# Optimization experiments

Hardware: AMD Instinct MI355X
Metric: run time of the kernel (lower is better)

Reference implementation:

```python
import jax, jax.numpy as jnp
import numpy as np
from jax import lax

B, C_IN, N, K = 4, 128, 4096, 16
C_OUT = 256
EPS = 1e-5


def setup_inputs() -> dict:
    key = jax.random.key(0)
    k1, k2, k3, k4, k5 = jax.random.split(key, 5)
    x = jax.random.normal(k1, (B, C_IN, N, 1), dtype=jnp.float32)
    y = jax.random.normal(k2, (B, C_IN, N, 1), dtype=jnp.float32)
    edge_index = jax.random.randint(k3, (2, B, N, K), 0, N)
    # Conv2d(in=2*C_IN, out=C_OUT, kernel 3x3), kaiming-ish scale
    fan_in = 2 * C_IN * 9
    conv_w = jax.random.normal(k4, (C_OUT, 2 * C_IN, 3, 3), dtype=jnp.float32) * (2.0 / fan_in) ** 0.5
    conv_b = jnp.zeros((C_OUT,), dtype=jnp.float32)
    gamma = jnp.ones((C_OUT,), dtype=jnp.float32)
    beta = jnp.zeros((C_OUT,), dtype=jnp.float32)
    _ = k5
    return {"x": x, "y": y, "edge_index": edge_index,
            "conv_w": conv_w, "conv_b": conv_b, "gamma": gamma, "beta": beta}


def _batched_index_select(feat, idx):
    # feat: [B, C, N, 1], idx: [B, N, K] -> [B, C, N, K]
    fs = feat[..., 0]  # [B, C, N]
    return jax.vmap(lambda fb, ib: fb[:, ib])(fs, idx)


def reference(x, y, edge_index, conv_w, conv_b, gamma, beta):
    x_i = _batched_index_select(x, edge_index[1])        # [B, C, N, K]
    x_j = _batched_index_select(y, edge_index[0])        # [B, C, N, K]
    h = jnp.concatenate([x_i, x_j - x_i], axis=1)        # [B, 2C, N, K]
    out = lax.conv_general_dilated(
        h, conv_w, window_strides=(1, 1), padding=((1, 1), (1, 1)),
        dimension_numbers=("NCHW", "OIHW", "NCHW"))
    out = out + conv_b[None, :, None, None]
    # BatchNorm2d in training mode: biased batch statistics per channel
    mean = jnp.mean(out, axis=(0, 2, 3), keepdims=True)
    var = jnp.mean((out - mean) ** 2, axis=(0, 2, 3), keepdims=True)
    out = gamma[None, :, None, None] * (out - mean) * lax.rsqrt(var + EPS) + beta[None, :, None, None]
    out = jax.nn.relu(out)
    return jnp.max(out, axis=-1, keepdims=True)          # [B, C_OUT, N, 1]
```

## Files before the change

kernel.cpp:

```cpp
#include <hip/hip_runtime.h>

typedef unsigned short u16;
typedef unsigned int u32;
typedef __attribute__((ext_vector_type(8))) u16 u16x8;
typedef __attribute__((ext_vector_type(8))) __bf16 bf16x8;
typedef __attribute__((ext_vector_type(4))) float f32x4;

#define CIN 128
#define NB 4
#define NN 4096
#define KPTS 16
#define COUT 256
#define POSB 65536
#define TOTPOS 262144
#define CK 2304

__device__ __forceinline__ float bf2f(u16 u){ return __uint_as_float(((u32)u)<<16); }
__device__ __forceinline__ u16 f2bf(float f){
  u32 u = __float_as_uint(f);
  u32 r = (u + 0x7fffu + ((u>>16)&1u)) >> 16;
  return (u16)r;
}

__global__ void pack_w_kernel(const float* __restrict__ w, u16* __restrict__ wp){
  int t = blockIdx.x*256 + threadIdx.x;
  if (t >= COUT*CK) return;
  int co = t / CK; int r = t - co*CK; int tap = r >> 8; int c = r & 255;
  float v;
  if (c < 128)
    v = w[(co*256 + c)*9 + tap] - w[(co*256 + 128 + c)*9 + tap];
  else
    v = w[(co*256 + c)*9 + tap];
  wp[t] = f2bf(v);
}

__global__ void transpose_cast_kernel(const float* __restrict__ x, const float* __restrict__ y,
                                      u16* __restrict__ xt, u16* __restrict__ yt){
  __shared__ u16 tile[2][32][65];
  int n0 = blockIdx.x*64, c0 = blockIdx.y*32, b = blockIdx.z;
  int t = threadIdx.x;
  int tn = t & 63, tc = t >> 6;
  #pragma unroll
  for (int i=0;i<8;++i){
    int c = tc*8 + i;
    size_t src = ((size_t)(b*CIN + c0 + c))*NN + n0 + tn;
    tile[0][c][tn] = f2bf(x[src]);
    tile[1][c][tn] = f2bf(y[src]);
  }
  __syncthreads();
  int tcc = t & 31, tnn = t >> 5;
  #pragma unroll
  for (int i=0;i<8;++i){
    int n = tnn*8 + i;
    size_t dst = ((size_t)(b*NN + n0 + n))*CIN + c0 + tcc;
    xt[dst] = tile[0][tcc][n];
    yt[dst] = tile[1][tcc][n];
  }
}

#define SWZ(row, chunk) (((row)*32) + ((((chunk) ^ (((row)>>1)&3))) << 3))

__global__ __launch_bounds__(256, 2) void conv_gemm_kernel(const u16* __restrict__ wp,
    const int* __restrict__ e, const u16* __restrict__ xt, const u16* __restrict__ yt,
    const u16* __restrict__ zrow, const float* __restrict__ bias,
    float* __restrict__ ssum, float* __restrict__ ssq, float* __restrict__ maxout){
  __shared__ u16 als[3*8192];
  __shared__ u16 pnl[2*6144];

  int ptile = blockIdx.x;
  int p0 = ptile * 128;
  int b = p0 >> 16;
  int pib0 = p0 & (POSB-1);
  int nb0 = pib0 >> 4;

  int t = threadIdx.x;
  int lane = t & 63, wave = t >> 6;
  int wr = wave >> 1, wc = wave & 1;
  int l15 = lane & 15, l4 = lane >> 4;

  const u16* xb = xt + ((size_t)b)*NN*CIN;
  const u16* yb = yt + ((size_t)b)*NN*CIN;

  int rr = wave*64 + (lane>>2);
  int r0 = rr, r1 = rr+16, r2 = rr+32, r3 = rr+48;
  int ch0 = (lane&3) ^ ((r0>>1)&3);
  int ch1 = (lane&3) ^ ((r1>>1)&3);
  int ch2 = (lane&3) ^ ((r2>>1)&3);
  int ch3 = (lane&3) ^ ((r3>>1)&3);
  int wuni = __builtin_amdgcn_readfirstlane(wave);
  int wu  = wuni*2048;
  int wu2 = wuni*512;
  const u16* pA0 = wp + (size_t)r0*CK + ch0*8;
  const u16* pA1 = wp + (size_t)r1*CK + ch1*8;
  const u16* pA2 = wp + (size_t)r2*CK + ch2*8;
  const u16* pA3 = wp + (size_t)r3*CK + ch3*8;

  const u16 *xp[3], *yp[3];
  { int tq4 = t >> 2;
    #pragma unroll
    for (int i=0;i<3;++i){
      int row = i*64 + tq4;
      int lc = (t&3) ^ ((row>>1)&3);
      int q = (row*57) >> 10;
      int kk = row - q*18 - 1;
      int n2 = nb0 - 1 + q;
      bool valid = (row < 180) && ((unsigned)n2 < (unsigned)NN) && ((unsigned)kk < (unsigned)KPTS);
      int j0 = 0, j1 = 0;
      if (valid){ int eo = b*POSB + n2*16 + kk; j0 = e[eo]; j1 = e[TOTPOS + eo]; }
      xp[i] = (valid ? xb + (size_t)j1*CIN : zrow) + lc*8;
      yp[i] = (valid ? yb + (size_t)j0*CIN : zrow) + lc*8;
    }
  }

  auto G16 = [&](const u16* g, const u16* l){
    __builtin_amdgcn_global_load_lds((const __attribute__((address_space(1))) u32*)g,
                                     (__attribute__((address_space(3))) u32*)l, 16, 0, 0);
  };

  f32x4 acc[8][4];
  #pragma unroll
  for (int i=0;i<8;++i)
    #pragma unroll
    for (int j=0;j<4;++j) acc[i][j] = (f32x4){0.f,0.f,0.f,0.f};

  G16(xp[0],    &pnl[wu2]);
  G16(xp[1],    &pnl[2048+wu2]);
  G16(xp[2],    &pnl[4096+wu2]);
  G16(xp[0]+32, &pnl[6144+wu2]);
  G16(xp[1]+32, &pnl[6144+2048+wu2]);
  G16(xp[2]+32, &pnl[6144+4096+wu2]);
  #pragma unroll
  for (int s=0; s<2; ++s){
    G16(pA0+s*256, &als[s*8192+wu]);
    G16(pA1+s*256, &als[s*8192+wu+512]);
    G16(pA2+s*256, &als[s*8192+wu+1024]);
    G16(pA3+s*256, &als[s*8192+wu+1536]);
  }

  int aoff[8];
  #pragma unroll
  for (int f=0; f<8; ++f) aoff[f] = SWZ(wr*128 + f*16 + l15, l4);
  int wc72l15 = wc*72 + l15;

  #define STEP(TAU) { \
    if ((TAU)==1) asm volatile("s_waitcnt vmcnt(7)\n\ts_barrier" ::: "memory"); \
    else          asm volatile("s_waitcnt vmcnt(4)\n\ts_barrier" ::: "memory"); \
    bf16x8 af[8], bv[4]; \
    { const int abase = ((TAU)%3)*8192; \
      _Pragma("unroll") \
      for (int f=0; f<8; ++f) af[f] = *(bf16x8*)&als[abase + aoff[f]]; } \
    { const u16* pb = pnl + (c&1)*6144; \
      const int kbc = ((TAU)/3)*18 + ((TAU)%3); \
      _Pragma("unroll") \
      for (int f=0; f<4; ++f){ int r = wc72l15 + kbc + f*18; \
        bv[f] = *(bf16x8*)&pb[r*32 + ((l4 ^ ((r>>1)&3))<<3)]; } } \
    if ((TAU)==0){ int cc=(c+1)&7; int co32=(cc&3)*32; \
      const u16* s0=(cc<4?xp[0]:yp[0])+co32; \
      const u16* s1=(cc<4?xp[1]:yp[1])+co32; \
      const u16* s2=(cc<4?xp[2]:yp[2])+co32; \
      int pd=((c+1)&1)*6144; \
      G16(s0,&pnl[pd+wu2]); G16(s1,&pnl[pd+2048+wu2]); G16(s2,&pnl[pd+4096+wu2]); } \
    { const int chs = (c + (((TAU)>=7)?1:0)) & 7; \
      const int koff = ((((TAU)+2)%9)*256) + (chs<<5); \
      const int sbase = (((TAU)+2)%3)*8192; \
      G16(pA0 + koff, &als[sbase + wu]); \
      G16(pA1 + koff, &als[sbase + wu + 512]); \
      G16(pA2 + koff, &als[sbase + wu + 1024]); \
      G16(pA3 + koff, &als[sbase + wu + 1536]); } \
    __builtin_amdgcn_s_setprio(1); \
    _Pragma("unroll") \
    for (int fm=0; fm<8; ++fm) \
      _Pragma("unroll") \
      for (int fn=0; fn<4; ++fn) \
        acc[fm][fn] = __builtin_amdgcn_mfma_f32_16x16x32_bf16(af[fm], bv[fn], acc[fm][fn], 0, 0, 0); \
    __builtin_amdgcn_s_setprio(0); \
  }

  for (int c = 0; c < 8; ++c){
    STEP(0) STEP(1) STEP(2) STEP(3) STEP(4) STEP(5) STEP(6) STEP(7) STEP(8)
  }
  #undef STEP

  asm volatile("s_waitcnt vmcnt(0)\n\ts_barrier" ::: "memory");

  float* fs = (float*)&als[0];
  fs[t] = 0.f; fs[256 + t] = 0.f;
  __syncthreads();

  #pragma unroll
  for (int fm=0; fm<8; ++fm){
    #pragma unroll
    for (int j=0; j<4; ++j){
      int ch = wr*128 + fm*16 + l4*4 + j;
      float bv2 = bias[ch];
      float s = 0.f, q = 0.f;
      float mv[4];
      #pragma unroll
      for (int fn=0; fn<4; ++fn){
        float v = acc[fm][fn][j] + bv2;
        s += v; q += v*v; mv[fn] = v;
      }
      #pragma unroll
      for (int o=1; o<16; o<<=1){
        s += __shfl_xor(s, o, 64);
        q += __shfl_xor(q, o, 64);
        #pragma unroll
        for (int fn=0; fn<4; ++fn) mv[fn] = fmaxf(mv[fn], __shfl_xor(mv[fn], o, 64));
      }
      if (l15 == 0){
        atomicAdd(&fs[ch], s);
        atomicAdd(&fs[256 + ch], q);
        size_t rowb = ((size_t)(b*COUT + ch)) << 12;
        #pragma unroll
        for (int fn=0; fn<4; ++fn)
          maxout[rowb + nb0 + wc*4 + fn] = mv[fn];
      }
    }
  }
  __syncthreads();
  atomicAdd(&ssum[t], fs[t]);
  atomicAdd(&ssq[t],  fs[256 + t]);
}

__global__ void finalize_stats_kernel(const float* __restrict__ ssum, const float* __restrict__ ssq,
                                      const float* __restrict__ gamma, const float* __restrict__ beta,
                                      float* __restrict__ scale, float* __restrict__ shift){
  int co = threadIdx.x;
  float inv = 1.0f / (float)TOTPOS;
  float mean = ssum[co]*inv;
  float var = ssq[co]*inv - mean*mean;
  float sc = gamma[co] * rsqrtf(var + 1e-5f);
  scale[co] = sc;
  shift[co] = beta[co] - mean*sc;
}

__global__ void bn_finish_kernel(float* __restrict__ out, const float* __restrict__ scale,
                                 const float* __restrict__ shift){
  int t = blockIdx.x*256 + threadIdx.x;
  int co = (t >> 12) & 255;
  float v = out[t];
  out[t] = fmaxf(fmaf(scale[co], v, shift[co]), 0.f);
}

extern "C" void kernel_launch(void* const* d_in, const int* in_sizes, int n_in,
                              void* d_out, int out_size, void* d_ws, size_t ws_size,
                              hipStream_t stream){
  const float* x = (const float*)d_in[0];
  const float* y = (const float*)d_in[1];
  const int*   e = (const int*)d_in[2];
  const float* w = (const float*)d_in[3];
  const float* bias = (const float*)d_in[4];
  const float* gamma = (const float*)d_in[5];
  const float* beta  = (const float*)d_in[6];
  float* out = (float*)d_out;

  char* ws = (char*)d_ws;
  u16*   wp    = (u16*)(ws);
  float* ssum  = (float*)(ws + 1179648);
  float* ssq   = (float*)(ws + 1180672);
  u16*   zrow  = (u16*)(ws + 1181696);
  float* scale = (float*)(ws + 1182720);
  float* shift = (float*)(ws + 1183744);
  u16*   xt    = (u16*)(ws + 1184768);
  u16*   yt    = (u16*)(ws + 5379072);

  hipMemsetAsync(ssum, 0, 3072, stream);

  pack_w_kernel<<<2304, 256, 0, stream>>>(w, wp);
  dim3 tg(NN/64, CIN/32, NB);
  transpose_cast_kernel<<<tg, 256, 0, stream>>>(x, y, xt, yt);
  conv_gemm_kernel<<<2048, 256, 0, stream>>>(wp, e, xt, yt, zrow, bias, ssum, ssq, out);
  finalize_stats_kernel<<<1, COUT, 0, stream>>>(ssum, ssq, gamma, beta, scale, shift);
  bn_finish_kernel<<<out_size/256, 256, 0, stream>>>(out, scale, shift);
}
```

Baseline: 324.0 us.

## Double-buffer MFMA fragments in registers and deepen LDS prefetch to three stages

The conv GEMM main loop now reads the next step's A and B fragments from LDS into a second register set while the current step's MFMAs run, ping-ponging between two fragment buffers. The global-to-LDS prefetch distance grows from two to three stages, so all three A slots are preloaded and the slot/offset arithmetic shifts accordingly. The loop over channel chunks is unrolled by two so the panel buffer pointers become compile-time selections. This aims to hide LDS read latency behind the matrix math, at the cost of more fragment registers and extra lgkmcnt waits at each barrier.

```diff
diff --git a/kernel.cpp b/kernel.cpp
--- a/kernel.cpp
+++ b/kernel.cpp
@@ -130,7 +130,7 @@
   G16(xp[1]+32, &pnl[6144+2048+wu2]);
   G16(xp[2]+32, &pnl[6144+4096+wu2]);
   #pragma unroll
-  for (int s=0; s<2; ++s){
+  for (int s=0; s<3; ++s){
     G16(pA0+s*256, &als[s*8192+wu]);
     G16(pA1+s*256, &als[s*8192+wu+512]);
     G16(pA2+s*256, &als[s*8192+wu+1024]);
@@ -142,27 +142,29 @@
   for (int f=0; f<8; ++f) aoff[f] = SWZ(wr*128 + f*16 + l15, l4);
   int wc72l15 = wc*72 + l15;
 
-  #define STEP(TAU) { \
-    if ((TAU)==1) asm volatile("s_waitcnt vmcnt(7)\n\ts_barrier" ::: "memory"); \
-    else          asm volatile("s_waitcnt vmcnt(4)\n\ts_barrier" ::: "memory"); \
-    bf16x8 af[8], bv[4]; \
-    { const int abase = ((TAU)%3)*8192; \
-      _Pragma("unroll") \
-      for (int f=0; f<8; ++f) af[f] = *(bf16x8*)&als[abase + aoff[f]]; } \
-    { const u16* pb = pnl + (c&1)*6144; \
-      const int kbc = ((TAU)/3)*18 + ((TAU)%3); \
-      _Pragma("unroll") \
-      for (int f=0; f<4; ++f){ int r = wc72l15 + kbc + f*18; \
-        bv[f] = *(bf16x8*)&pb[r*32 + ((l4 ^ ((r>>1)&3))<<3)]; } } \
+  bf16x8 f0_a[8], f0_b[4], f1_a[8], f1_b[4];
+
+  asm volatile("s_waitcnt vmcnt(8)\n\ts_barrier" ::: "memory");
+  #pragma unroll
+  for (int f=0; f<8; ++f) f0_a[f] = *(bf16x8*)&als[aoff[f]];
+  #pragma unroll
+  for (int f=0; f<4; ++f){
+    int r = wc72l15 + f*18;
+    f0_b[f] = *(bf16x8*)&pnl[r*32 + ((l4 ^ ((r>>1)&3))<<3)];
+  }
+
+  #define STEP(TAU, CUR, NXT) { \
+    if ((TAU)==1) asm volatile("s_waitcnt vmcnt(7)\n\ts_waitcnt lgkmcnt(0)\n\ts_barrier" ::: "memory"); \
+    else          asm volatile("s_waitcnt vmcnt(4)\n\ts_waitcnt lgkmcnt(0)\n\ts_barrier" ::: "memory"); \
     if ((TAU)==0){ int cc=(c+1)&7; int co32=(cc&3)*32; \
       const u16* s0=(cc<4?xp[0]:yp[0])+co32; \
       const u16* s1=(cc<4?xp[1]:yp[1])+co32; \
       const u16* s2=(cc<4?xp[2]:yp[2])+co32; \
       int pd=((c+1)&1)*6144; \
       G16(s0,&pnl[pd+wu2]); G16(s1,&pnl[pd+2048+wu2]); G16(s2,&pnl[pd+4096+wu2]); } \
-    { const int chs = (c + (((TAU)>=7)?1:0)) & 7; \
-      const int koff = ((((TAU)+2)%9)*256) + (chs<<5); \
-      const int sbase = (((TAU)+2)%3)*8192; \
+    { const int chs = (c + (((TAU)>=6)?1:0)) & 7; \
+      const int koff = ((((TAU)+3)%9)*256) + (chs<<5); \
+      const int sbase = ((TAU)%3)*8192; \
       G16(pA0 + koff, &als[sbase + wu]); \
       G16(pA1 + koff, &als[sbase + wu + 512]); \
       G16(pA2 + koff, &als[sbase + wu + 1024]); \
@@ -172,16 +174,40 @@
     for (int fm=0; fm<8; ++fm) \
       _Pragma("unroll") \
       for (int fn=0; fn<4; ++fn) \
-        acc[fm][fn] = __builtin_amdgcn_mfma_f32_16x16x32_bf16(af[fm], bv[fn], acc[fm][fn], 0, 0, 0); \
+        acc[fm][fn] = __builtin_amdgcn_mfma_f32_16x16x32_bf16(CUR##_a[fm], CUR##_b[fn], acc[fm][fn], 0, 0, 0); \
     __builtin_amdgcn_s_setprio(0); \
-  }
-
-  for (int c = 0; c < 8; ++c){
-    STEP(0) STEP(1) STEP(2) STEP(3) STEP(4) STEP(5) STEP(6) STEP(7) STEP(8)
+    { const int abase = (((TAU)+1)%3)*8192; \
+      _Pragma("unroll") \
+      for (int f=0; f<8; ++f) NXT##_a[f] = *(bf16x8*)&als[abase + aoff[f]]; } \
+    { const u16* pb = ((TAU)==8) ? pbN : pbC; \
+      const int tn = ((TAU)+1)%9; \
+      const int kbc = (tn/3)*18 + (tn%3); \
+      _Pragma("unroll") \
+      for (int f=0; f<4; ++f){ int r = wc72l15 + kbc + f*18; \
+        NXT##_b[f] = *(bf16x8*)&pb[r*32 + ((l4 ^ ((r>>1)&3))<<3)]; } } \
+  }
+
+  for (int cp = 0; cp < 8; cp += 2){
+    {
+      int c = cp;
+      const u16* pbC = pnl;
+      const u16* pbN = pnl + 6144;
+      STEP(0, f0, f1)  STEP(1, f1, f0)  STEP(2, f0, f1)
+      STEP(3, f1, f0)  STEP(4, f0, f1)  STEP(5, f1, f0)
+      STEP(6, f0, f1)  STEP(7, f1, f0)  STEP(8, f0, f1)
+    }
+    {
+      int c = cp + 1;
+      const u16* pbC = pnl + 6144;
+      const u16* pbN = pnl;
+      STEP(0, f1, f0)  STEP(1, f0, f1)  STEP(2, f1, f0)
+      STEP(3, f0, f1)  STEP(4, f1, f0)  STEP(5, f0, f1)
+      STEP(6, f1, f0)  STEP(7, f0, f1)  STEP(8, f1, f0)
+    }
   }
   #undef STEP
 
-  asm volatile("s_waitcnt vmcnt(0)\n\ts_barrier" ::: "memory");
+  asm volatile("s_waitcnt vmcnt(0)\n\ts_waitcnt lgkmcnt(0)\n\ts_barrier" ::: "memory");
 
   float* fs = (float*)&als[0];
   fs[t] = 0.f; fs[256 + t] = 0.f;
```

After: 336.0 us. 3.7% more time.

## Split MFMA step into halves and prefetch next step's LDS fragments

Applied to the files above, without the earlier changes.

Restructures the GEMM main-loop step into two half-phases. Each phase issues 16 MFMAs while LDS reads for the other half of the A fragments, and for the next step's A and B fragments, are in flight. The B fragments and first A half are preloaded before the loop. The aim is to hide LDS read latency behind matrix-core work, a ping-pong style schedule. In exchange each step now has four barriers instead of one and the vmcnt/buffer-index bookkeeping is more complex, which adds sync overhead and correctness risk around the stage-buffer reuse.

```diff
diff --git a/kernel.cpp b/kernel.cpp
--- a/kernel.cpp
+++ b/kernel.cpp
@@ -142,18 +142,19 @@
   for (int f=0; f<8; ++f) aoff[f] = SWZ(wr*128 + f*16 + l15, l4);
   int wc72l15 = wc*72 + l15;
 
+  bf16x8 af[8], bv[4];
+
+  asm volatile("s_waitcnt vmcnt(4)" ::: "memory");
+  asm volatile("s_barrier" ::: "memory");
+  #pragma unroll
+  for (int f=0; f<4; ++f) af[f] = *(bf16x8*)&als[aoff[f]];
+  #pragma unroll
+  for (int f=0; f<4; ++f){
+    int r = wc72l15 + f*18;
+    bv[f] = *(bf16x8*)&pnl[r*32 + ((l4 ^ ((r>>1)&3))<<3)];
+  }
+
   #define STEP(TAU) { \
-    if ((TAU)==1) asm volatile("s_waitcnt vmcnt(7)\n\ts_barrier" ::: "memory"); \
-    else          asm volatile("s_waitcnt vmcnt(4)\n\ts_barrier" ::: "memory"); \
-    bf16x8 af[8], bv[4]; \
-    { const int abase = ((TAU)%3)*8192; \
-      _Pragma("unroll") \
-      for (int f=0; f<8; ++f) af[f] = *(bf16x8*)&als[abase + aoff[f]]; } \
-    { const u16* pb = pnl + (c&1)*6144; \
-      const int kbc = ((TAU)/3)*18 + ((TAU)%3); \
-      _Pragma("unroll") \
-      for (int f=0; f<4; ++f){ int r = wc72l15 + kbc + f*18; \
-        bv[f] = *(bf16x8*)&pb[r*32 + ((l4 ^ ((r>>1)&3))<<3)]; } } \
     if ((TAU)==0){ int cc=(c+1)&7; int co32=(cc&3)*32; \
       const u16* s0=(cc<4?xp[0]:yp[0])+co32; \
       const u16* s1=(cc<4?xp[1]:yp[1])+co32; \
@@ -167,13 +168,40 @@
       G16(pA1 + koff, &als[sbase + wu + 512]); \
       G16(pA2 + koff, &als[sbase + wu + 1024]); \
       G16(pA3 + koff, &als[sbase + wu + 1536]); } \
+    asm volatile("s_barrier" ::: "memory"); \
+    asm volatile("s_waitcnt lgkmcnt(0)" ::: "memory"); \
     __builtin_amdgcn_s_setprio(1); \
     _Pragma("unroll") \
-    for (int fm=0; fm<8; ++fm) \
+    for (int fm=0; fm<4; ++fm) \
       _Pragma("unroll") \
       for (int fn=0; fn<4; ++fn) \
         acc[fm][fn] = __builtin_amdgcn_mfma_f32_16x16x32_bf16(af[fm], bv[fn], acc[fm][fn], 0, 0, 0); \
     __builtin_amdgcn_s_setprio(0); \
+    asm volatile("s_barrier" ::: "memory"); \
+    { const int abase = ((TAU)%3)*8192; \
+      _Pragma("unroll") \
+      for (int f=4; f<8; ++f) af[f] = *(bf16x8*)&als[abase + aoff[f]]; } \
+    if ((TAU)==0) asm volatile("s_waitcnt vmcnt(7)" ::: "memory"); \
+    else          asm volatile("s_waitcnt vmcnt(4)" ::: "memory"); \
+    asm volatile("s_barrier" ::: "memory"); \
+    asm volatile("s_waitcnt lgkmcnt(0)" ::: "memory"); \
+    __builtin_amdgcn_s_setprio(1); \
+    _Pragma("unroll") \
+    for (int fm=4; fm<8; ++fm) \
+      _Pragma("unroll") \
+      for (int fn=0; fn<4; ++fn) \
+        acc[fm][fn] = __builtin_amdgcn_mfma_f32_16x16x32_bf16(af[fm], bv[fn], acc[fm][fn], 0, 0, 0); \
+    __builtin_amdgcn_s_setprio(0); \
+    asm volatile("s_barrier" ::: "memory"); \
+    { const int abase = (((TAU)+1)%3)*8192; \
+      _Pragma("unroll") \
+      for (int f=0; f<4; ++f) af[f] = *(bf16x8*)&als[abase + aoff[f]]; \
+      const u16* pb = pnl + (((((TAU)==8) ? (c+1) : c)) & 1)*6144; \
+      const int tn = ((TAU)+1)%9; \
+      const int kbc = (tn/3)*18 + (tn%3); \
+      _Pragma("unroll") \
+      for (int f=0; f<4; ++f){ int r = wc72l15 + kbc + f*18; \
+        bv[f] = *(bf16x8*)&pb[r*32 + ((l4 ^ ((r>>1)&3))<<3)]; } } \
   }
 
   for (int c = 0; c < 8; ++c){
@@ -181,7 +209,9 @@
   }
   #undef STEP
 
-  asm volatile("s_waitcnt vmcnt(0)\n\ts_barrier" ::: "memory");
+  asm volatile("s_waitcnt vmcnt(0)" ::: "memory");
+  asm volatile("s_waitcnt lgkmcnt(0)" ::: "memory");
+  asm volatile("s_barrier" ::: "memory");
 
   float* fs = (float*)&als[0];
   fs[t] = 0.f; fs[256 + t] = 0.f;
```

After: 341.9 us. 1.06x slower.

## Split conv GEMM tile across eight waves with halved per-wave accumulators

Applied to the files above, without the earlier changes.

Doubles the GEMM block to 512 threads, so each wave computes a 64x64 output sub-tile instead of 128x64, cutting accumulators per thread from 128 to 64 floats. A-tile and gather-panel loads are redistributed to two 16-byte loads per thread. The activation panel buffers grow to 256 rows, and the wait counts are adjusted to match. Launch bounds now request 4 blocks per CU, which caps registers tightly and risks spills. The larger LDS footprint may also prevent that occupancy from being reached.

```diff
diff --git a/kernel.cpp b/kernel.cpp
--- a/kernel.cpp
+++ b/kernel.cpp
@@ -60,12 +60,12 @@
 
 #define SWZ(row, chunk) (((row)*32) + ((((chunk) ^ (((row)>>1)&3))) << 3))
 
-__global__ __launch_bounds__(256, 2) void conv_gemm_kernel(const u16* __restrict__ wp,
+__global__ __launch_bounds__(512, 4) void conv_gemm_kernel(const u16* __restrict__ wp,
     const int* __restrict__ e, const u16* __restrict__ xt, const u16* __restrict__ yt,
     const u16* __restrict__ zrow, const float* __restrict__ bias,
     float* __restrict__ ssum, float* __restrict__ ssq, float* __restrict__ maxout){
   __shared__ u16 als[3*8192];
-  __shared__ u16 pnl[2*6144];
+  __shared__ u16 pnl[2*8192];
 
   int ptile = blockIdx.x;
   int p0 = ptile * 128;
@@ -81,25 +81,19 @@
   const u16* xb = xt + ((size_t)b)*NN*CIN;
   const u16* yb = yt + ((size_t)b)*NN*CIN;
 
-  int rr = wave*64 + (lane>>2);
-  int r0 = rr, r1 = rr+16, r2 = rr+32, r3 = rr+48;
-  int ch0 = (lane&3) ^ ((r0>>1)&3);
-  int ch1 = (lane&3) ^ ((r1>>1)&3);
-  int ch2 = (lane&3) ^ ((r2>>1)&3);
-  int ch3 = (lane&3) ^ ((r3>>1)&3);
-  int wuni = __builtin_amdgcn_readfirstlane(wave);
-  int wu  = wuni*2048;
-  int wu2 = wuni*512;
-  const u16* pA0 = wp + (size_t)r0*CK + ch0*8;
-  const u16* pA1 = wp + (size_t)r1*CK + ch1*8;
-  const u16* pA2 = wp + (size_t)r2*CK + ch2*8;
-  const u16* pA3 = wp + (size_t)r3*CK + ch3*8;
-
-  const u16 *xp[3], *yp[3];
+  int rA0 = wave*16 + (lane>>2);
+  int rA1 = rA0 + 128;
+  int chA0 = (lane&3) ^ ((rA0>>1)&3);
+  int chA1 = (lane&3) ^ ((rA1>>1)&3);
+  int wu = __builtin_amdgcn_readfirstlane(wave) * 512;
+  const u16* pA0 = wp + (size_t)rA0*CK + chA0*8;
+  const u16* pA1 = wp + (size_t)rA1*CK + chA1*8;
+
+  const u16 *xp[2], *yp[2];
   { int tq4 = t >> 2;
     #pragma unroll
-    for (int i=0;i<3;++i){
-      int row = i*64 + tq4;
+    for (int j=0;j<2;++j){
+      int row = j*128 + tq4;
       int lc = (t&3) ^ ((row>>1)&3);
       int q = (row*57) >> 10;
       int kk = row - q*18 - 1;
@@ -107,8 +101,8 @@
       bool valid = (row < 180) && ((unsigned)n2 < (unsigned)NN) && ((unsigned)kk < (unsigned)KPTS);
       int j0 = 0, j1 = 0;
       if (valid){ int eo = b*POSB + n2*16 + kk; j0 = e[eo]; j1 = e[TOTPOS + eo]; }
-      xp[i] = (valid ? xb + (size_t)j1*CIN : zrow) + lc*8;
-      yp[i] = (valid ? yb + (size_t)j0*CIN : zrow) + lc*8;
+      xp[j] = (valid ? xb + (size_t)j1*CIN : zrow) + lc*8;
+      yp[j] = (valid ? yb + (size_t)j0*CIN : zrow) + lc*8;
     }
   }
 
@@ -117,39 +111,35 @@
                                      (__attribute__((address_space(3))) u32*)l, 16, 0, 0);
   };
 
-  f32x4 acc[8][4];
-  #pragma unroll
-  for (int i=0;i<8;++i)
+  f32x4 acc[4][4];
+  #pragma unroll
+  for (int i=0;i<4;++i)
     #pragma unroll
     for (int j=0;j<4;++j) acc[i][j] = (f32x4){0.f,0.f,0.f,0.f};
 
-  G16(xp[0],    &pnl[wu2]);
-  G16(xp[1],    &pnl[2048+wu2]);
-  G16(xp[2],    &pnl[4096+wu2]);
-  G16(xp[0]+32, &pnl[6144+wu2]);
-  G16(xp[1]+32, &pnl[6144+2048+wu2]);
-  G16(xp[2]+32, &pnl[6144+4096+wu2]);
+  G16(xp[0],    &pnl[wu]);
+  G16(xp[1],    &pnl[4096+wu]);
+  G16(xp[0]+32, &pnl[8192+wu]);
+  G16(xp[1]+32, &pnl[8192+4096+wu]);
   #pragma unroll
   for (int s=0; s<2; ++s){
     G16(pA0+s*256, &als[s*8192+wu]);
-    G16(pA1+s*256, &als[s*8192+wu+512]);
-    G16(pA2+s*256, &als[s*8192+wu+1024]);
-    G16(pA3+s*256, &als[s*8192+wu+1536]);
-  }
-
-  int aoff[8];
-  #pragma unroll
-  for (int f=0; f<8; ++f) aoff[f] = SWZ(wr*128 + f*16 + l15, l4);
+    G16(pA1+s*256, &als[s*8192+4096+wu]);
+  }
+
+  int aoff[4];
+  #pragma unroll
+  for (int f=0; f<4; ++f) aoff[f] = SWZ(wr*64 + f*16 + l15, l4);
   int wc72l15 = wc*72 + l15;
 
   #define STEP(TAU) { \
-    if ((TAU)==1) asm volatile("s_waitcnt vmcnt(7)\n\ts_barrier" ::: "memory"); \
-    else          asm volatile("s_waitcnt vmcnt(4)\n\ts_barrier" ::: "memory"); \
-    bf16x8 af[8], bv[4]; \
+    if ((TAU)==1) asm volatile("s_waitcnt vmcnt(4)\n\ts_barrier" ::: "memory"); \
+    else          asm volatile("s_waitcnt vmcnt(2)\n\ts_barrier" ::: "memory"); \
+    bf16x8 af[4], bv[4]; \
     { const int abase = ((TAU)%3)*8192; \
       _Pragma("unroll") \
-      for (int f=0; f<8; ++f) af[f] = *(bf16x8*)&als[abase + aoff[f]]; } \
-    { const u16* pb = pnl + (c&1)*6144; \
+      for (int f=0; f<4; ++f) af[f] = *(bf16x8*)&als[abase + aoff[f]]; } \
+    { const u16* pb = pnl + (c&1)*8192; \
       const int kbc = ((TAU)/3)*18 + ((TAU)%3); \
       _Pragma("unroll") \
       for (int f=0; f<4; ++f){ int r = wc72l15 + kbc + f*18; \
@@ -157,19 +147,16 @@
     if ((TAU)==0){ int cc=(c+1)&7; int co32=(cc&3)*32; \
       const u16* s0=(cc<4?xp[0]:yp[0])+co32; \
       const u16* s1=(cc<4?xp[1]:yp[1])+co32; \
-      const u16* s2=(cc<4?xp[2]:yp[2])+co32; \
-      int pd=((c+1)&1)*6144; \
-      G16(s0,&pnl[pd+wu2]); G16(s1,&pnl[pd+2048+wu2]); G16(s2,&pnl[pd+4096+wu2]); } \
+      int pd=((c+1)&1)*8192; \
+      G16(s0,&pnl[pd+wu]); G16(s1,&pnl[pd+4096+wu]); } \
     { const int chs = (c + (((TAU)>=7)?1:0)) & 7; \
       const int koff = ((((TAU)+2)%9)*256) + (chs<<5); \
       const int sbase = (((TAU)+2)%3)*8192; \
       G16(pA0 + koff, &als[sbase + wu]); \
-      G16(pA1 + koff, &als[sbase + wu + 512]); \
-      G16(pA2 + koff, &als[sbase + wu + 1024]); \
-      G16(pA3 + koff, &als[sbase + wu + 1536]); } \
+      G16(pA1 + koff, &als[sbase + 4096 + wu]); } \
     __builtin_amdgcn_s_setprio(1); \
     _Pragma("unroll") \
-    for (int fm=0; fm<8; ++fm) \
+    for (int fm=0; fm<4; ++fm) \
       _Pragma("unroll") \
       for (int fn=0; fn<4; ++fn) \
         acc[fm][fn] = __builtin_amdgcn_mfma_f32_16x16x32_bf16(af[fm], bv[fn], acc[fm][fn], 0, 0, 0); \
@@ -184,14 +171,14 @@
   asm volatile("s_waitcnt vmcnt(0)\n\ts_barrier" ::: "memory");
 
   float* fs = (float*)&als[0];
-  fs[t] = 0.f; fs[256 + t] = 0.f;
+  fs[t] = 0.f;
   __syncthreads();
 
   #pragma unroll
-  for (int fm=0; fm<8; ++fm){
+  for (int fm=0; fm<4; ++fm){
     #pragma unroll
     for (int j=0; j<4; ++j){
-      int ch = wr*128 + fm*16 + l4*4 + j;
+      int ch = wr*64 + fm*16 + l4*4 + j;
       float bv2 = bias[ch];
       float s = 0.f, q = 0.f;
       float mv[4];
@@ -218,8 +205,8 @@
     }
   }
   __syncthreads();
-  atomicAdd(&ssum[t], fs[t]);
-  atomicAdd(&ssq[t],  fs[256 + t]);
+  if (t < 256) atomicAdd(&ssum[t], fs[t]);
+  else         atomicAdd(&ssq[t-256], fs[t]);
 }
 
 __global__ void finalize_stats_kernel(const float* __restrict__ ssum, const float* __restrict__ ssq,
@@ -269,7 +256,7 @@
   pack_w_kernel<<<2304, 256, 0, stream>>>(w, wp);
   dim3 tg(NN/64, CIN/32, NB);
   transpose_cast_kernel<<<tg, 256, 0, stream>>>(x, y, xt, yt);
-  conv_gemm_kernel<<<2048, 256, 0, stream>>>(wp, e, xt, yt, zrow, bias, ssum, ssq, out);
+  conv_gemm_kernel<<<2048, 512, 0, stream>>>(wp, e, xt, yt, zrow, bias, ssum, ssq, out);
   finalize_stats_kernel<<<1, COUT, 0, stream>>>(ssum, ssq, gamma, beta, scale, shift);
   bn_finish_kernel<<<out_size/256, 256, 0, stream>>>(out, scale, shift);
 }
```

Measured after the change: 439.6 us. +35.7%, slower.
